# Kernel tuning notes

Measured on AMD Instinct MI355X. Metric: run time of the kernel, lower is better.

Reference implementation:

```python
import jax, jax.numpy as jnp
import numpy as np
import math

# ---- physical constants (QMAV) ----
MASS = 1.5
GRAV = 9.81
_J_NP = np.diag([0.0211, 0.0219, 0.0366]).astype(np.float32)
J = jnp.asarray(_J_NP)
J_INV = jnp.asarray(np.linalg.inv(_J_NP).astype(np.float32))
KD_X = KD_Y = KD_Z = 0.10   # linear drag coeffs
K_H = 0.01                   # horizontal-velocity lift coeff
O_MIN, O_MAX = 0.0, 1000.0   # rotor speed limits [rad/s]
KT, KM, ARM = 1.0e-5, 1.0e-7, 0.15
_G_VEC = jnp.array([0.0, 0.0, GRAV], jnp.float32).reshape(1, 3, 1)  # NED, down positive


def make_G1():
    # [T, Mx, My, Mz] = G_1 @ [o1^2, o2^2, o3^2, o4^2], X-configuration mixer
    c = ARM * KT * math.sqrt(2.0) / 2.0
    return np.array([
        [KT,  KT,  KT,  KT],
        [-c,   c,   c,  -c],
        [-c,  -c,   c,   c],
        [-KM,  KM, -KM,  KM],
    ], dtype=np.float32)


def quat_to_rot(q):
    # q: [B,4,1] = (ew,ex,ey,ez) -> body-to-inertial rotation [B,3,3]
    ew, ex, ey, ez = q[:, 0, 0], q[:, 1, 0], q[:, 2, 0], q[:, 3, 0]
    r = jnp.stack([
        ew**2 + ex**2 - ey**2 - ez**2, 2*(ex*ey - ew*ez), 2*(ex*ez + ew*ey),
        2*(ex*ey + ew*ez), ew**2 - ex**2 + ey**2 - ez**2, 2*(ey*ez - ew*ex),
        2*(ex*ez - ew*ey), 2*(ey*ez + ew*ex), ew**2 - ex**2 - ey**2 + ez**2,
    ], axis=-1)
    return r.reshape(-1, 3, 3)


def quat_to_euler(q):
    ew, ex, ey, ez = q[:, 0:1, :], q[:, 1:2, :], q[:, 2:3, :], q[:, 3:4, :]
    phi = jnp.arctan2(2*(ew*ex + ey*ez), ew**2 + ez**2 - ex**2 - ey**2)
    theta = jnp.arcsin(jnp.clip(2*(ew*ey - ex*ez), -1.0, 1.0))
    psi = jnp.arctan2(2*(ew*ez + ex*ey), ew**2 + ex**2 - ey**2 - ez**2)
    return phi, theta, psi


def rigid_body_deriv(x, u):
    # x: [B,13,1] = [pos(3), v_world(3), quat(4), omega(3)]; u: [B,6,1] = [f_inertial(3), moment_body(3)]
    v = x[:, 3:6, :]
    q = x[:, 6:10, :]
    w = x[:, 10:13, :]
    f_i = u[:, 0:3, :]
    m_b = u[:, 3:6, :]
    pos_dot = v
    v_dot = f_i / MASS + _G_VEC
    ew, ex, ey, ez = q[:, 0:1, :], q[:, 1:2, :], q[:, 2:3, :], q[:, 3:4, :]
    p, qq, r = w[:, 0:1, :], w[:, 1:2, :], w[:, 2:3, :]
    q_dot = 0.5 * jnp.concatenate([
        -ex*p - ey*qq - ez*r,
         ew*p + ey*r - ez*qq,
         ew*qq - ex*r + ez*p,
         ew*r + ex*qq - ey*p,
    ], axis=1)
    Jw = jnp.einsum('ij,bjk->bik', J, w)
    w_dot = jnp.einsum('ij,bjk->bik', J_INV, m_b - jnp.cross(w, Jw, axis=1))
    return jnp.concatenate([pos_dot, v_dot, q_dot, w_dot], axis=1)


def rk4_step(x, u, dt):
    k1 = rigid_body_deriv(x, u)
    k2 = rigid_body_deriv(x + 0.5 * dt * k1, u)
    k3 = rigid_body_deriv(x + 0.5 * dt * k2, u)
    k4 = rigid_body_deriv(x + dt * k3, u)
    return x + (dt / 6.0) * (k1 + 2*k2 + 2*k3 + k4)


def setup_inputs() -> dict:
    key = jax.random.key(0)
    k1, k2 = jax.random.split(key)
    B = 1 << 20
    state = jax.random.normal(k1, (B, 32, 1), dtype=jnp.float32)
    # normalize the quaternion slice so the initial attitude is valid
    q = state[:, 9:13, :]
    state = state.at[:, 9:13, :].set(q / jnp.sqrt(jnp.sum(q**2, axis=1, keepdims=True)))
    delta = jax.random.uniform(k2, (B, 4, 1), dtype=jnp.float32) * O_MAX
    G_1 = jnp.asarray(make_G1())
    return {"state": state, "delta": delta, "G_1": G_1, "dt": 0.02}


def reference(state, delta, G_1, dt):
    # ---- forces / moments + wind-related state ----
    d = jnp.clip(delta, O_MIN, O_MAX)
    tt = jnp.einsum('ij,bjk->bik', G_1, d**2)  # [B,4,1] = [T, Mx, My, Mz]
    T = tt[:, 0:1, :]; Mx = tt[:, 1:2, :]; My = tt[:, 2:3, :]; Mz = tt[:, 3:4, :]
    R = quat_to_rot(state[:, 9:13, :])
    V_wind_b = jnp.einsum('bji,bjk->bik', R, state[:, 28:31, :])  # R^T @ wind_inertial
    u_r = state[:, 16:17, :] - V_wind_b[:, 0:1, :]
    v_r = state[:, 17:18, :] - V_wind_b[:, 1:2, :]
    w_r = state[:, 18:19, :] - V_wind_b[:, 2:3, :]
    Va = jnp.sqrt(u_r**2 + v_r**2 + w_r**2)
    u_safe = jnp.where(u_r == 0.0, 1.0, u_r)
    alpha = jnp.where(u_r == 0.0, math.pi / 2, jnp.arctan2(w_r, u_safe))
    Va_safe = jnp.where(Va == 0.0, 1.0, Va)
    beta = jnp.where(Va == 0.0, 0.0, jnp.arcsin(jnp.clip(v_r / Va_safe, -1.0, 1.0)))
    state = state.at[:, 22:23, :].set(Va)
    state = state.at[:, 24:25, :].set(alpha)
    state = state.at[:, 25:26, :].set(beta)
    fx = -KD_X * u_r
    fy = -KD_Y * v_r
    fz = -T - KD_Z * w_r + K_H * (u_r**2 + v_r**2)
    f_i = R @ jnp.concatenate([fx, fy, fz], axis=1)
    fm = jnp.concatenate([f_i, Mx, My, Mz], axis=1)  # [B,6,1]
    # ---- rigid-body RK4 integration ----
    ode_state = jnp.concatenate(
        [state[:, 3:6, :], state[:, 13:16, :], state[:, 9:13, :], state[:, 19:22, :]], axis=1)
    new = rk4_step(ode_state, fm, dt)
    qn = new[:, 6:10, :]
    qn = qn / jnp.sqrt(jnp.sum(qn**2, axis=1, keepdims=True))
    state = state.at[:, 3:6, :].set(new[:, 0:3, :])
    state = state.at[:, 13:16, :].set(new[:, 3:6, :])
    state = state.at[:, 9:13, :].set(qn)
    state = state.at[:, 19:22, :].set(new[:, 10:13, :])
    # ---- other derived states (R from the pre-update quaternion, as in original) ----
    phi, theta, psi = quat_to_euler(state[:, 9:13, :])
    pdot = R @ state[:, 16:19, :]
    Vg = jnp.sqrt(jnp.sum(pdot**2, axis=(1, 2)))[:, None, None]
    Vg_safe = jnp.where(Vg == 0.0, 1.0, Vg)
    gamma = jnp.arcsin(jnp.clip(pdot[:, 2:3, :] / Vg_safe, -1.0, 1.0))
    chi = jnp.arctan2(pdot[:, 1:2, :], pdot[:, 0:1, :])
    state = state.at[:, 6:7, :].set(phi)
    state = state.at[:, 7:8, :].set(theta)
    state = state.at[:, 8:9, :].set(psi)
    state = state.at[:, 23:24, :].set(Vg)
    state = state.at[:, 26:27, :].set(gamma)
    state = state.at[:, 27:28, :].set(chi)
    return state
```

## Files before the change

### kernel.cpp

```cpp
#include <hip/hip_runtime.h>
#include <math.h>


#define INV_MASSF  (1.0f / 1.5f)
#define GRAVF      9.81f
#define KDF        0.1f
#define KHF        0.01f
#define JXF        0.0211f
#define JYF        0.0219f
#define JZF        0.0366f
#define JIXF       (1.0f / 0.0211f)
#define JIYF       (1.0f / 0.0219f)
#define JIZF       (1.0f / 0.0366f)
#define PI_2F      1.57079632679489661923f

#define ROWS    256
#define WROWS   64

__device__ __forceinline__ float clamp1(float x) {
    return fminf(fmaxf(x, -1.0f), 1.0f);
}

__device__ __forceinline__ void qw_deriv(const float x[7],
                                         float mx, float my, float mz,
                                         float k[7]) {
    const float ew = x[0], ex = x[1], ey = x[2], ez = x[3];
    const float p = x[4], q = x[5], r = x[6];
    k[0] = 0.5f * (-ex * p - ey * q - ez * r);
    k[1] = 0.5f * ( ew * p + ey * r - ez * q);
    k[2] = 0.5f * ( ew * q - ex * r + ez * p);
    k[3] = 0.5f * ( ew * r + ex * q - ey * p);
    const float Jwx = JXF * p, Jwy = JYF * q, Jwz = JZF * r;
    k[4] = (mx - (q * Jwz - r * Jwy)) * JIXF;
    k[5] = (my - (r * Jwx - p * Jwz)) * JIYF;
    k[6] = (mz - (p * Jwy - q * Jwx)) * JIZF;
}

__device__ __forceinline__ void qd_compute(const float s[32], float4 dl,
                                           const float* __restrict__ G1,
                                           float dt, float o[32]) {
    float T, Mx, My, Mz;
    {
        float d0 = fminf(fmaxf(dl.x, 0.0f), 1000.0f);
        float d1 = fminf(fmaxf(dl.y, 0.0f), 1000.0f);
        float d2 = fminf(fmaxf(dl.z, 0.0f), 1000.0f);
        float d3 = fminf(fmaxf(dl.w, 0.0f), 1000.0f);
        d0 *= d0; d1 *= d1; d2 *= d2; d3 *= d3;
        const float4* g4 = (const float4*)G1;
        const float4 g0 = g4[0], g1 = g4[1], g2 = g4[2], g3 = g4[3];
        T  = g0.x * d0 + g0.y * d1 + g0.z * d2 + g0.w * d3;
        Mx = g1.x * d0 + g1.y * d1 + g1.z * d2 + g1.w * d3;
        My = g2.x * d0 + g2.y * d1 + g2.z * d2 + g2.w * d3;
        Mz = g3.x * d0 + g3.y * d1 + g3.z * d2 + g3.w * d3;
    }

    const float ew = s[9], ex = s[10], ey = s[11], ez = s[12];

    const float r00 = ew*ew + ex*ex - ey*ey - ez*ez;
    const float r01 = 2.0f * (ex*ey - ew*ez);
    const float r02 = 2.0f * (ex*ez + ew*ey);
    const float r10 = 2.0f * (ex*ey + ew*ez);
    const float r11 = ew*ew - ex*ex + ey*ey - ez*ez;
    const float r12 = 2.0f * (ey*ez - ew*ex);
    const float r20 = 2.0f * (ex*ez - ew*ey);
    const float r21 = 2.0f * (ey*ez + ew*ex);
    const float r22 = ew*ew - ex*ex - ey*ey + ez*ez;

    const float vwb0 = r00 * s[28] + r10 * s[29] + r20 * s[30];
    const float vwb1 = r01 * s[28] + r11 * s[29] + r21 * s[30];
    const float vwb2 = r02 * s[28] + r12 * s[29] + r22 * s[30];

    const float u_r = s[16] - vwb0;
    const float v_r = s[17] - vwb1;
    const float w_r = s[18] - vwb2;
    const float Va = sqrtf(u_r * u_r + v_r * v_r + w_r * w_r);
    const float alpha = (u_r == 0.0f) ? PI_2F : atan2f(w_r, u_r);
    const float beta  = (Va == 0.0f) ? 0.0f : asinf(clamp1(v_r / Va));

    const float fx = -KDF * u_r;
    const float fy = -KDF * v_r;
    const float fz = -T - KDF * w_r + KHF * (u_r * u_r + v_r * v_r);
    const float vd0 = (r00 * fx + r01 * fy + r02 * fz) * INV_MASSF;
    const float vd1 = (r10 * fx + r11 * fy + r12 * fz) * INV_MASSF;
    const float vd2 = (r20 * fx + r21 * fy + r22 * fz) * INV_MASSF + GRAVF;

    const float vn0 = s[13] + dt * vd0;
    const float vn1 = s[14] + dt * vd1;
    const float vn2 = s[15] + dt * vd2;
    const float hdt2 = 0.5f * dt * dt;
    const float pn0 = s[3] + dt * s[13] + hdt2 * vd0;
    const float pn1 = s[4] + dt * s[14] + hdt2 * vd1;
    const float pn2 = s[5] + dt * s[15] + hdt2 * vd2;

    const float h2 = 0.5f * dt;
    float x0[7] = {ew, ex, ey, ez, s[19], s[20], s[21]};
    float k[7], acc[7], xt[7], xn[7];
    qw_deriv(x0, Mx, My, Mz, k);
    #pragma unroll
    for (int i = 0; i < 7; ++i) { acc[i] = k[i]; xt[i] = x0[i] + h2 * k[i]; }
    qw_deriv(xt, Mx, My, Mz, k);
    #pragma unroll
    for (int i = 0; i < 7; ++i) { acc[i] += 2.0f * k[i]; xt[i] = x0[i] + h2 * k[i]; }
    qw_deriv(xt, Mx, My, Mz, k);
    #pragma unroll
    for (int i = 0; i < 7; ++i) { acc[i] += 2.0f * k[i]; xt[i] = x0[i] + dt * k[i]; }
    qw_deriv(xt, Mx, My, Mz, k);
    const float dt6 = dt / 6.0f;
    #pragma unroll
    for (int i = 0; i < 7; ++i) xn[i] = x0[i] + dt6 * (acc[i] + k[i]);

    float qw2 = xn[0], qx2 = xn[1], qy2 = xn[2], qz2 = xn[3];
    const float qi = 1.0f / sqrtf(qw2*qw2 + qx2*qx2 + qy2*qy2 + qz2*qz2);
    qw2 *= qi; qx2 *= qi; qy2 *= qi; qz2 *= qi;

    const float phi = atan2f(2.0f * (qw2 * qx2 + qy2 * qz2),
                             qw2*qw2 + qz2*qz2 - qx2*qx2 - qy2*qy2);
    const float theta = asinf(clamp1(2.0f * (qw2 * qy2 - qx2 * qz2)));
    const float psi = atan2f(2.0f * (qw2 * qz2 + qx2 * qy2),
                             qw2*qw2 + qx2*qx2 - qy2*qy2 - qz2*qz2);

    const float p0 = r00 * s[16] + r01 * s[17] + r02 * s[18];
    const float p1 = r10 * s[16] + r11 * s[17] + r12 * s[18];
    const float p2 = r20 * s[16] + r21 * s[17] + r22 * s[18];
    const float Vg = sqrtf(p0 * p0 + p1 * p1 + p2 * p2);
    const float vgs = (Vg == 0.0f) ? 1.0f : Vg;
    const float gamma = asinf(clamp1(p2 / vgs));
    const float chi = atan2f(p1, p0);

    o[0] = s[0]; o[1] = s[1]; o[2] = s[2];
    o[3] = pn0; o[4] = pn1; o[5] = pn2;
    o[6] = phi; o[7] = theta; o[8] = psi;
    o[9] = qw2; o[10] = qx2; o[11] = qy2; o[12] = qz2;
    o[13] = vn0; o[14] = vn1; o[15] = vn2;
    o[16] = s[16]; o[17] = s[17]; o[18] = s[18];
    o[19] = xn[4]; o[20] = xn[5]; o[21] = xn[6];
    o[22] = Va; o[23] = Vg;
    o[24] = alpha; o[25] = beta;
    o[26] = gamma; o[27] = chi;
    o[28] = s[28]; o[29] = s[29]; o[30] = s[30]; o[31] = s[31];
}

__global__ __launch_bounds__(ROWS, 5) void qd_dynamics_kernel(
    const float* __restrict__ state,
    const float* __restrict__ delta,
    const float* __restrict__ G1,
    const float* __restrict__ dtp,
    float* __restrict__ out,
    int B)
{
    __shared__ __align__(16) float lds[ROWS * 32];

    const int tid  = threadIdx.x;
    const int lane = tid & 63;
    const int wv   = tid >> 6;
    const int row0 = blockIdx.x * ROWS;
    const int wrow0 = row0 + wv * WROWS;
    float* lw = &lds[wv * (WROWS * 32)];
    const bool full = (row0 + ROWS) <= B;

    const float dt = dtp[0];

    float s[32], o[32];
    float4 dl;

    if (full) {
        const float* gb = state + (size_t)wrow0 * 32;
        #pragma unroll
        for (int i = 0; i < 8; ++i) {
            const int slot = i * 64 + lane;
            const int r  = slot >> 3;
            const int c4 = slot & 7;
            const int sc = c4 ^ (r & 7);
            __builtin_amdgcn_global_load_lds(
                (const __attribute__((address_space(1))) void*)
                    (gb + (size_t)r * 32 + sc * 4),
                (__attribute__((address_space(3))) void*)(lw + i * 256),
                16, 0, 0);
        }
        dl = ((const float4*)delta)[row0 + tid];
        asm volatile("s_waitcnt vmcnt(0)" ::: "memory");

        #pragma unroll
        for (int lc = 0; lc < 8; ++lc)
            ((float4*)s)[lc] =
                *(const float4*)&lw[(lane * 8 + (lc ^ (lane & 7))) * 4];
    } else {
        const int b = row0 + tid;
        const int bb = (b < B) ? b : (B - 1);
        const float4* sp = (const float4*)(state + (size_t)bb * 32);
        #pragma unroll
        for (int i = 0; i < 8; ++i) ((float4*)s)[i] = sp[i];
        dl = ((const float4*)delta)[bb];
    }

    qd_compute(s, dl, G1, dt, o);

    if (full) {
        #pragma unroll
        for (int lc = 0; lc < 8; ++lc)
            *(float4*)&lw[(lane * 8 + (lc ^ (lane & 7))) * 4] =
                ((const float4*)o)[lc];
        float4* ob = (float4*)(out + (size_t)wrow0 * 32);
        #pragma unroll
        for (int i = 0; i < 8; ++i) {
            const int slot = i * 64 + lane;
            const int r  = slot >> 3;
            const int c4 = slot & 7;
            const int p  = r * 8 + (c4 ^ (r & 7));
            ob[slot] = *(const float4*)&lw[p * 4];
        }
    } else {
        const int b = row0 + tid;
        if (b < B) {
            float4* op = (float4*)(out + (size_t)b * 32);
            #pragma unroll
            for (int i = 0; i < 8; ++i) op[i] = ((const float4*)o)[i];
        }
    }
}

extern "C" void kernel_launch(void* const* d_in, const int* in_sizes, int n_in,
                              void* d_out, int out_size, void* d_ws, size_t ws_size,
                              hipStream_t stream) {
    const float* state = (const float*)d_in[0];
    const float* delta = (const float*)d_in[1];
    const float* G1    = (const float*)d_in[2];
    const float* dtp   = (const float*)d_in[3];
    float* out = (float*)d_out;
    const int B = in_sizes[0] / 32;
    const int grid = (B + ROWS - 1) / ROWS;
    hipLaunchKernelGGL(qd_dynamics_kernel, dim3(grid), dim3(ROWS), 0, stream,
                       state, delta, G1, dtp, out, B);
}
```

Measured before the change: 248.8 us.

## Convert to persistent grid with double-buffered LDS prefetch of state tiles

Result: no change. 250.0 us (+0.5%).

```diff
diff --git a/kernel.cpp b/kernel.cpp
--- a/kernel.cpp
+++ b/kernel.cpp
@@ -15,7 +15,7 @@
 #define PI_2F      1.57079632679489661923f
 
 #define ROWS    256
-#define WROWS   64
+#define GRID_T  512
 
 __device__ __forceinline__ float clamp1(float x) {
     return fminf(fmaxf(x, -1.0f), 1.0f);
@@ -37,22 +37,18 @@
 }
 
 __device__ __forceinline__ void qd_compute(const float s[32], float4 dl,
-                                           const float* __restrict__ G1,
+                                           float4 g0, float4 g1,
+                                           float4 g2, float4 g3,
                                            float dt, float o[32]) {
-    float T, Mx, My, Mz;
-    {
-        float d0 = fminf(fmaxf(dl.x, 0.0f), 1000.0f);
-        float d1 = fminf(fmaxf(dl.y, 0.0f), 1000.0f);
-        float d2 = fminf(fmaxf(dl.z, 0.0f), 1000.0f);
-        float d3 = fminf(fmaxf(dl.w, 0.0f), 1000.0f);
-        d0 *= d0; d1 *= d1; d2 *= d2; d3 *= d3;
-        const float4* g4 = (const float4*)G1;
-        const float4 g0 = g4[0], g1 = g4[1], g2 = g4[2], g3 = g4[3];
-        T  = g0.x * d0 + g0.y * d1 + g0.z * d2 + g0.w * d3;
-        Mx = g1.x * d0 + g1.y * d1 + g1.z * d2 + g1.w * d3;
-        My = g2.x * d0 + g2.y * d1 + g2.z * d2 + g2.w * d3;
-        Mz = g3.x * d0 + g3.y * d1 + g3.z * d2 + g3.w * d3;
-    }
+    float d0 = fminf(fmaxf(dl.x, 0.0f), 1000.0f);
+    float d1 = fminf(fmaxf(dl.y, 0.0f), 1000.0f);
+    float d2 = fminf(fmaxf(dl.z, 0.0f), 1000.0f);
+    float d3 = fminf(fmaxf(dl.w, 0.0f), 1000.0f);
+    d0 *= d0; d1 *= d1; d2 *= d2; d3 *= d3;
+    const float T  = g0.x * d0 + g0.y * d1 + g0.z * d2 + g0.w * d3;
+    const float Mx = g1.x * d0 + g1.y * d1 + g1.z * d2 + g1.w * d3;
+    const float My = g2.x * d0 + g2.y * d1 + g2.z * d2 + g2.w * d3;
+    const float Mz = g3.x * d0 + g3.y * d1 + g3.z * d2 + g3.w * d3;
 
     const float ew = s[9], ex = s[10], ey = s[11], ez = s[12];
 
@@ -140,7 +136,25 @@
     o[28] = s[28]; o[29] = s[29]; o[30] = s[30]; o[31] = s[31];
 }
 
-__global__ __launch_bounds__(ROWS, 5) void qd_dynamics_kernel(
+__device__ __forceinline__ void stage_tile(const float* __restrict__ state,
+                                           int tile, int wv, int lane,
+                                           float* buf) {
+    const float* gb = state + ((size_t)tile * 256 + (size_t)wv * 64) * 32;
+    #pragma unroll
+    for (int i = 0; i < 8; ++i) {
+        const int slot = i * 64 + lane;
+        const int r  = slot >> 3;
+        const int c4 = slot & 7;
+        const int sc = c4 ^ (r & 7);
+        __builtin_amdgcn_global_load_lds(
+            (const __attribute__((address_space(1))) void*)
+                (gb + (size_t)r * 32 + sc * 4),
+            (__attribute__((address_space(3))) void*)(buf + i * 256),
+            16, 0, 0);
+    }
+}
+
+__global__ __launch_bounds__(ROWS, 2) void qd_dynamics_kernel(
     const float* __restrict__ state,
     const float* __restrict__ delta,
     const float* __restrict__ G1,
@@ -148,70 +162,80 @@
     float* __restrict__ out,
     int B)
 {
-    __shared__ __align__(16) float lds[ROWS * 32];
+    __shared__ __align__(16) float lds[ROWS * 64];
 
     const int tid  = threadIdx.x;
     const int lane = tid & 63;
     const int wv   = tid >> 6;
-    const int row0 = blockIdx.x * ROWS;
-    const int wrow0 = row0 + wv * WROWS;
-    float* lw = &lds[wv * (WROWS * 32)];
-    const bool full = (row0 + ROWS) <= B;
-
+    float* lw = &lds[wv * 4096];
+
+    const int ntiles = B >> 8;
+    const int stride = (int)gridDim.x;
     const float dt = dtp[0];
 
-    float s[32], o[32];
-    float4 dl;
-
-    if (full) {
-        const float* gb = state + (size_t)wrow0 * 32;
-        #pragma unroll
-        for (int i = 0; i < 8; ++i) {
-            const int slot = i * 64 + lane;
-            const int r  = slot >> 3;
-            const int c4 = slot & 7;
-            const int sc = c4 ^ (r & 7);
-            __builtin_amdgcn_global_load_lds(
-                (const __attribute__((address_space(1))) void*)
-                    (gb + (size_t)r * 32 + sc * 4),
-                (__attribute__((address_space(3))) void*)(lw + i * 256),
-                16, 0, 0);
+    const float4* g4 = (const float4*)G1;
+    const float4 g0 = g4[0], g1 = g4[1], g2 = g4[2], g3 = g4[3];
+
+    float4 dl_cur = make_float4(0.f, 0.f, 0.f, 0.f);
+    float4 dl_next = dl_cur;
+
+    const int t0 = (int)blockIdx.x;
+    if (t0 < ntiles) {
+        stage_tile(state, t0, wv, lane, lw);
+        dl_cur = ((const float4*)delta)[t0 * 256 + wv * 64 + lane];
+    }
+
+    int phase = 0;
+    for (int t = t0; t < ntiles; t += stride) {
+        float* bc = lw + (phase << 11);
+        float* bn = lw + ((phase ^ 1) << 11);
+        const int tn = t + stride;
+
+        if (tn < ntiles) {
+            stage_tile(state, tn, wv, lane, bn);
+            dl_next = ((const float4*)delta)[tn * 256 + wv * 64 + lane];
+            asm volatile("s_waitcnt vmcnt(9)" ::: "memory");
+        } else {
+            asm volatile("s_waitcnt vmcnt(0)" ::: "memory");
         }
-        dl = ((const float4*)delta)[row0 + tid];
-        asm volatile("s_waitcnt vmcnt(0)" ::: "memory");
-
+
+        float s[32], o[32];
         #pragma unroll
         for (int lc = 0; lc < 8; ++lc)
             ((float4*)s)[lc] =
-                *(const float4*)&lw[(lane * 8 + (lc ^ (lane & 7))) * 4];
-    } else {
-        const int b = row0 + tid;
-        const int bb = (b < B) ? b : (B - 1);
-        const float4* sp = (const float4*)(state + (size_t)bb * 32);
-        #pragma unroll
-        for (int i = 0; i < 8; ++i) ((float4*)s)[i] = sp[i];
-        dl = ((const float4*)delta)[bb];
-    }
-
-    qd_compute(s, dl, G1, dt, o);
-
-    if (full) {
+                *(const float4*)&bc[(lane * 8 + (lc ^ (lane & 7))) * 4];
+
+        qd_compute(s, dl_cur, g0, g1, g2, g3, dt, o);
+
         #pragma unroll
         for (int lc = 0; lc < 8; ++lc)
-            *(float4*)&lw[(lane * 8 + (lc ^ (lane & 7))) * 4] =
+            *(float4*)&bc[(lane * 8 + (lc ^ (lane & 7))) * 4] =
                 ((const float4*)o)[lc];
-        float4* ob = (float4*)(out + (size_t)wrow0 * 32);
+        float4* ob = (float4*)(out + ((size_t)t * 256 + (size_t)wv * 64) * 32);
         #pragma unroll
         for (int i = 0; i < 8; ++i) {
             const int slot = i * 64 + lane;
             const int r  = slot >> 3;
             const int c4 = slot & 7;
             const int p  = r * 8 + (c4 ^ (r & 7));
-            ob[slot] = *(const float4*)&lw[p * 4];
+            ob[slot] = *(const float4*)&bc[p * 4];
         }
-    } else {
-        const int b = row0 + tid;
+
+        dl_cur = dl_next;
+        phase ^= 1;
+        __builtin_amdgcn_sched_barrier(0);
+    }
+
+    const int rem0 = ntiles << 8;
+    if (rem0 < B && (int)blockIdx.x == (ntiles % stride)) {
+        const int b = rem0 + tid;
         if (b < B) {
+            float s[32], o[32];
+            const float4* sp = (const float4*)(state + (size_t)b * 32);
+            #pragma unroll
+            for (int i = 0; i < 8; ++i) ((float4*)s)[i] = sp[i];
+            const float4 dl = ((const float4*)delta)[b];
+            qd_compute(s, dl, g0, g1, g2, g3, dt, o);
             float4* op = (float4*)(out + (size_t)b * 32);
             #pragma unroll
             for (int i = 0; i < 8; ++i) op[i] = ((const float4*)o)[i];
@@ -228,7 +252,8 @@
     const float* dtp   = (const float*)d_in[3];
     float* out = (float*)d_out;
     const int B = in_sizes[0] / 32;
-    const int grid = (B + ROWS - 1) / ROWS;
+    const int ntiles = B >> 8;
+    int grid = (ntiles < GRID_T) ? (ntiles > 0 ? ntiles : 1) : GRID_T;
     hipLaunchKernelGGL(qd_dynamics_kernel, dim3(grid), dim3(ROWS), 0, stream,
                        state, delta, G1, dtp, out, B);
 }
```
